# Kernel optimization log

Hardware: AMD Instinct MI355X
Metric: run time of the kernel (lower is better)

The kernel has to match this reference:

```python
import jax, jax.numpy as jnp
import numpy as np

BS, NV, NC = 16, 2048, 16
MAX_CLUSTER = 128


def _block_target(cluster_sizes, n, dtype):
    # Faithful to the original torch code, which does `prev = n` (NOT prev += n):
    # block k occupies [start_k, start_k + n_k) with start_0 = 0, start_k = n_{k-1}.
    starts = jnp.concatenate([jnp.zeros_like(cluster_sizes[:, :1]), cluster_sizes[:, :-1]], axis=1)  # (bs, K)
    ends = starts + cluster_sizes  # (bs, K)
    idx = jnp.arange(n)  # (n,)
    # membership M[b,k,i] = start_k <= i < end_k
    M = ((idx[None, None, :] >= starts[:, :, None]) & (idx[None, None, :] < ends[:, :, None]))  # (bs,K,n)
    Mf = M.astype(dtype)
    # target[b,i,j] = 1 if any cluster k covers both i and j (overlaps collapse to 1, matching .set of ones)
    cov = jnp.einsum('bki,bkj->bij', Mf, Mf)  # (bs,n,n)
    return (cov > 0).astype(dtype)


def setup_inputs() -> dict:
    key = jax.random.key(0)
    k1, k2 = jax.random.split(key)
    raw_scores = jax.random.normal(k1, (BS, NV, NV), dtype=jnp.float32)
    cluster_sizes = jax.random.randint(k2, (BS, NC), 0, MAX_CLUSTER).astype(jnp.int64)
    return {"raw_scores": raw_scores, "cluster_sizes": cluster_sizes}


def reference(raw_scores, cluster_sizes):
    target = _block_target(cluster_sizes, raw_scores.shape[-1], raw_scores.dtype)
    # nn.MSELoss(reduction='mean')
    return jnp.mean((raw_scores - target) ** 2)
```

## Files before the change

kernel.cpp:

```cpp
#include <hip/hip_runtime.h>

#define NV 2048
#define BS 16
#define NC 16

#define TOTAL_F 67108864LL
#define N4 (TOTAL_F / 4)

#define NBLK 2048
#define STR  (N4 / NBLK / 256 ? (long long)NBLK * 256 : 0)
#define ITERS 32

__global__ __launch_bounds__(256) void k_main(const float* __restrict__ x,
                                              const int* __restrict__ cs,
                                              float* __restrict__ partial) {
    int bid = blockIdx.x;
    int t = threadIdx.x;
    const float4* x4 = (const float4*)x;
    const long long stride = (long long)NBLK * 256;
    long long base = (long long)bid * 256 + t;

    float a0 = 0.f, a1 = 0.f, a2 = 0.f, a3 = 0.f;
#pragma unroll
    for (int it = 0; it < ITERS; it += 4) {
        float4 v0 = x4[base + (long long)(it + 0) * stride];
        float4 v1 = x4[base + (long long)(it + 1) * stride];
        float4 v2 = x4[base + (long long)(it + 2) * stride];
        float4 v3 = x4[base + (long long)(it + 3) * stride];
        a0 += v0.x * v0.x + v0.y * v0.y + v0.z * v0.z + v0.w * v0.w;
        a1 += v1.x * v1.x + v1.y * v1.y + v1.z * v1.z + v1.w * v1.w;
        a2 += v2.x * v2.x + v2.y * v2.y + v2.z * v2.z + v2.w * v2.w;
        a3 += v3.x * v3.x + v3.y * v3.y + v3.z * v3.z + v3.w * v3.w;
    }
    float s = (a0 + a1) + (a2 + a3);

    int b  = bid >> 7;
    int i0 = (bid & 127) * 2;
    __shared__ int st_[NC], en_[NC];
    if (t < NC) {
        int sz = cs[b * NC + t];
        int st = (t == 0) ? 0 : cs[b * NC + t - 1];
        st_[t] = st;
        en_[t] = st + sz;
    }
    __syncthreads();
    unsigned m0 = 0, m1 = 0, mj = 0;
#pragma unroll
    for (int k = 0; k < NC; ++k) {
        int st = st_[k], en = en_[k];
        if (t  >= st && t  < en) mj |= 1u << k;
        if (i0 >= st && i0 < en) m0 |= 1u << k;
        if (i0 + 1 >= st && i0 + 1 < en) m1 |= 1u << k;
    }
    const float* xb = x + (long long)b * NV * NV;
    if (m0 & mj) s += 1.0f - 2.0f * xb[(long long)i0 * NV + t];
    if (m1 & mj) s += 1.0f - 2.0f * xb[(long long)(i0 + 1) * NV + t];

    for (int off = 32; off > 0; off >>= 1)
        s += __shfl_down(s, off, 64);
    __shared__ float wsum[4];
    if ((t & 63) == 0) wsum[t >> 6] = s;
    __syncthreads();
    if (t == 0) partial[bid] = wsum[0] + wsum[1] + wsum[2] + wsum[3];
}

__global__ __launch_bounds__(256) void k_final(const float* __restrict__ partial,
                                               float* __restrict__ out) {
    int t = threadIdx.x;
    float s = 0.f;
#pragma unroll
    for (int i = 0; i < NBLK / 256; ++i)
        s += partial[t + i * 256];
    for (int off = 32; off > 0; off >>= 1)
        s += __shfl_down(s, off, 64);
    __shared__ float wsum[4];
    if ((t & 63) == 0) wsum[t >> 6] = s;
    __syncthreads();
    if (t == 0)
        out[0] = (wsum[0] + wsum[1] + wsum[2] + wsum[3]) * (1.0f / (float)TOTAL_F);
}

extern "C" void kernel_launch(void* const* d_in, const int* in_sizes, int n_in,
                              void* d_out, int out_size, void* d_ws, size_t ws_size,
                              hipStream_t stream) {
    const float* raw_scores = (const float*)d_in[0];
    const int*   cluster_sz = (const int*)d_in[1];
    float* out = (float*)d_out;
    float* partial = (float*)d_ws;

    k_main<<<NBLK, 256, 0, stream>>>(raw_scores, cluster_sz, partial);
    k_final<<<1, 256, 0, stream>>>(partial, out);
}
```

Measured before the change: 51.79 us.

## Give each block a contiguous tile and fuse corner correction into streaming pass

Each block now streams a contiguous 128 KB chunk (32 float4 per thread) instead of grid-strided loads, using nontemporal loads for non-corner blocks. The blocks whose chunk covers the top-left 256x256 corner of a batch compute row and column cluster masks and apply the target correction from the values already loaded. This drops the separate re-read of corner rows that every block used to do, and avoids cache pollution on the stream. Corner blocks pay extra mask and setup work, which adds some load imbalance.

```diff
diff --git a/kernel.cpp b/kernel.cpp
--- a/kernel.cpp
+++ b/kernel.cpp
@@ -5,56 +5,94 @@
 #define NC 16
 
 #define TOTAL_F 67108864LL
-#define N4 (TOTAL_F / 4)
+#define NBLK 2048
+#define F4_PER_BLOCK 8192
 
-#define NBLK 2048
-#define STR  (N4 / NBLK / 256 ? (long long)NBLK * 256 : 0)
-#define ITERS 32
+typedef float fx4 __attribute__((ext_vector_type(4)));
+
 
 __global__ __launch_bounds__(256) void k_main(const float* __restrict__ x,
                                               const int* __restrict__ cs,
                                               float* __restrict__ partial) {
     int bid = blockIdx.x;
     int t = threadIdx.x;
-    const float4* x4 = (const float4*)x;
-    const long long stride = (long long)NBLK * 256;
-    long long base = (long long)bid * 256 + t;
+    const fx4* x4 = (const fx4*)x + (long long)bid * F4_PER_BLOCK;
 
-    float a0 = 0.f, a1 = 0.f, a2 = 0.f, a3 = 0.f;
+    bool corner = (bid & 127) < 16;
+    float s = 0.f;
+
+    if (!corner) {
+        float a[8] = {0.f, 0.f, 0.f, 0.f, 0.f, 0.f, 0.f, 0.f};
 #pragma unroll
-    for (int it = 0; it < ITERS; it += 4) {
-        float4 v0 = x4[base + (long long)(it + 0) * stride];
-        float4 v1 = x4[base + (long long)(it + 1) * stride];
-        float4 v2 = x4[base + (long long)(it + 2) * stride];
-        float4 v3 = x4[base + (long long)(it + 3) * stride];
-        a0 += v0.x * v0.x + v0.y * v0.y + v0.z * v0.z + v0.w * v0.w;
-        a1 += v1.x * v1.x + v1.y * v1.y + v1.z * v1.z + v1.w * v1.w;
-        a2 += v2.x * v2.x + v2.y * v2.y + v2.z * v2.z + v2.w * v2.w;
-        a3 += v3.x * v3.x + v3.y * v3.y + v3.z * v3.z + v3.w * v3.w;
+        for (int g = 0; g < 4; ++g) {
+            fx4 v[8];
+#pragma unroll
+            for (int u = 0; u < 8; ++u)
+                v[u] = __builtin_nontemporal_load(&x4[(g * 8 + u) * 256 + t]);
+#pragma unroll
+            for (int u = 0; u < 8; ++u)
+                a[u] += v[u].x * v[u].x + v[u].y * v[u].y + v[u].z * v[u].z + v[u].w * v[u].w;
+        }
+        s = ((a[0] + a[1]) + (a[2] + a[3])) + ((a[4] + a[5]) + (a[6] + a[7]));
+    } else {
+        int b = bid >> 7;
+        int r0 = (bid & 127) << 4;
+        __shared__ int st_[NC], en_[NC];
+        __shared__ unsigned rowm[16];
+        if (t < NC) {
+            int sz = cs[b * NC + t];
+            int st = (t == 0) ? 0 : cs[b * NC + t - 1];
+            st_[t] = st;
+            en_[t] = st + sz;
+        }
+        __syncthreads();
+        if (t < 16) {
+            int r = r0 + t;
+            unsigned m = 0;
+#pragma unroll
+            for (int k = 0; k < NC; ++k)
+                if (r >= st_[k] && r < en_[k]) m |= 1u << k;
+            rowm[t] = m;
+        }
+        unsigned cm0 = 0, cm1 = 0, cm2 = 0, cm3 = 0;
+        if (t < 64) {
+            int c = t * 4;
+#pragma unroll
+            for (int k = 0; k < NC; ++k) {
+                int st = st_[k], en = en_[k];
+                if (c     >= st && c     < en) cm0 |= 1u << k;
+                if (c + 1 >= st && c + 1 < en) cm1 |= 1u << k;
+                if (c + 2 >= st && c + 2 < en) cm2 |= 1u << k;
+                if (c + 3 >= st && c + 3 < en) cm3 |= 1u << k;
+            }
+        }
+        __syncthreads();
+
+        float a[8] = {0.f, 0.f, 0.f, 0.f, 0.f, 0.f, 0.f, 0.f};
+#pragma unroll
+        for (int g = 0; g < 4; ++g) {
+            fx4 v[8];
+#pragma unroll
+            for (int u = 0; u < 8; ++u)
+                v[u] = x4[(g * 8 + u) * 256 + t];
+#pragma unroll
+            for (int u = 0; u < 8; ++u)
+                a[u] += v[u].x * v[u].x + v[u].y * v[u].y + v[u].z * v[u].z + v[u].w * v[u].w;
+#pragma unroll
+            for (int u = 0; u < 8; ++u) {
+                int i = g * 8 + u;
+                if ((i & 1) == 0 && t < 64) {
+                    unsigned rm = rowm[i >> 1];
+                    fx4 vv = v[u];
+                    s += (rm & cm0) ? (1.f - 2.f * vv.x) : 0.f;
+                    s += (rm & cm1) ? (1.f - 2.f * vv.y) : 0.f;
+                    s += (rm & cm2) ? (1.f - 2.f * vv.z) : 0.f;
+                    s += (rm & cm3) ? (1.f - 2.f * vv.w) : 0.f;
+                }
+            }
+        }
+        s += ((a[0] + a[1]) + (a[2] + a[3])) + ((a[4] + a[5]) + (a[6] + a[7]));
     }
-    float s = (a0 + a1) + (a2 + a3);
-
-    int b  = bid >> 7;
-    int i0 = (bid & 127) * 2;
-    __shared__ int st_[NC], en_[NC];
-    if (t < NC) {
-        int sz = cs[b * NC + t];
-        int st = (t == 0) ? 0 : cs[b * NC + t - 1];
-        st_[t] = st;
-        en_[t] = st + sz;
-    }
-    __syncthreads();
-    unsigned m0 = 0, m1 = 0, mj = 0;
-#pragma unroll
-    for (int k = 0; k < NC; ++k) {
-        int st = st_[k], en = en_[k];
-        if (t  >= st && t  < en) mj |= 1u << k;
-        if (i0 >= st && i0 < en) m0 |= 1u << k;
-        if (i0 + 1 >= st && i0 + 1 < en) m1 |= 1u << k;
-    }
-    const float* xb = x + (long long)b * NV * NV;
-    if (m0 & mj) s += 1.0f - 2.0f * xb[(long long)i0 * NV + t];
-    if (m1 & mj) s += 1.0f - 2.0f * xb[(long long)(i0 + 1) * NV + t];
 
     for (int off = 32; off > 0; off >>= 1)
         s += __shfl_down(s, off, 64);
```

After: 47.28 us. 1.1x faster.
